# Kernel optimization log

Hardware: AMD Instinct MI355X
Metric: run time of the kernel (lower is better)

The kernel has to match this reference:

```python
import jax, jax.numpy as jnp
import numpy as np

B, T, C, H = 8, 2048, 1024, 64

def setup_inputs() -> dict:
    key = jax.random.key(0)
    k1, k2, k3, k4 = jax.random.split(key, 4)
    x = jax.random.normal(k1, (B, T, C), dtype=jnp.float32)
    s = 1.0 / np.sqrt(C)
    Wq = jax.random.normal(k2, (C, H), dtype=jnp.float32) * s
    Wk = jax.random.normal(k3, (C, H), dtype=jnp.float32) * s
    Wv = jax.random.normal(k4, (C, H), dtype=jnp.float32) * s
    return {"x": x, "Wq": Wq, "Wk": Wk, "Wv": Wv}

def reference(x, Wq, Wk, Wv):
    # single-head causal attention; note: scale uses sqrt(n_emb)=sqrt(C), as in source
    q = jnp.einsum('btc,ch->bth', x, Wq)
    k = jnp.einsum('btc,ch->bth', x, Wk)
    v = jnp.einsum('btc,ch->bth', x, Wv)
    wei = jnp.einsum('bth,bsh->bts', q, k) / jnp.sqrt(jnp.float32(C))  # [B,T,T]
    causal = jnp.tril(jnp.ones((T, T), dtype=bool))
    wei = jnp.where(causal, wei, jnp.float32(-jnp.inf))
    wei = jax.nn.softmax(wei, axis=-1)
    out = jnp.einsum('bts,bsh->bth', wei, v)  # [B,T,H]
    return out
```

## Files before the change

### kernel.cpp

```cpp
#include <hip/hip_runtime.h>

#define BT_ (8 * 2048)
#define T_  2048
#define H_  64

__global__ __launch_bounds__(256) void qkv_proj(
    const float* __restrict__ x,
    const float* __restrict__ Wq,
    const float* __restrict__ Wk,
    const float* __restrict__ Wv,
    float* __restrict__ qkv) {
  __shared__ float xT[32][68];
  __shared__ float wl[32][196];

  const int tid = threadIdx.x;
  const int tx = tid & 15;
  const int ty = tid >> 4;
  const int row0 = blockIdx.x * 64;

  float acc[4][12];
#pragma unroll
  for (int r = 0; r < 4; ++r)
#pragma unroll
    for (int c = 0; c < 12; ++c) acc[r][c] = 0.f;

  for (int kc = 0; kc < 1024; kc += 32) {
#pragma unroll
    for (int i = 0; i < 2; ++i) {
      int idx = tid + i * 256;
      int r = idx >> 3;
      int k4 = (idx & 7) * 4;
      const float4 v = *reinterpret_cast<const float4*>(
          &x[(size_t)(row0 + r) * 1024 + kc + k4]);
      xT[k4 + 0][r] = v.x;
      xT[k4 + 1][r] = v.y;
      xT[k4 + 2][r] = v.z;
      xT[k4 + 3][r] = v.w;
    }
    {
      const float* wp[3] = {Wq, Wk, Wv};
#pragma unroll
      for (int m = 0; m < 3; ++m) {
#pragma unroll
        for (int i = 0; i < 2; ++i) {
          int idx = tid + i * 256;
          int r = idx >> 4;
          int h4 = (idx & 15) * 4;
          const float4 v = *reinterpret_cast<const float4*>(
              &wp[m][(size_t)(kc + r) * 64 + h4]);
          *reinterpret_cast<float4*>(&wl[r][m * 64 + h4]) = v;
        }
      }
    }
    __syncthreads();

#pragma unroll
    for (int kk = 0; kk < 32; ++kk) {
      const float4 xv = *reinterpret_cast<const float4*>(&xT[kk][ty * 4]);
      const float4 w0 = *reinterpret_cast<const float4*>(&wl[kk][tx * 12 + 0]);
      const float4 w1 = *reinterpret_cast<const float4*>(&wl[kk][tx * 12 + 4]);
      const float4 w2 = *reinterpret_cast<const float4*>(&wl[kk][tx * 12 + 8]);
      const float xr[4] = {xv.x, xv.y, xv.z, xv.w};
      const float wr[12] = {w0.x, w0.y, w0.z, w0.w, w1.x, w1.y, w1.z, w1.w,
                            w2.x, w2.y, w2.z, w2.w};
#pragma unroll
      for (int r = 0; r < 4; ++r)
#pragma unroll
        for (int c = 0; c < 12; ++c)
          acc[r][c] = fmaf(xr[r], wr[c], acc[r][c]);
    }
    __syncthreads();
  }

#pragma unroll
  for (int r = 0; r < 4; ++r) {
#pragma unroll
    for (int g = 0; g < 3; ++g) {
      const int col = tx * 12 + g * 4;
      const int m = col >> 6;
      const int h = col & 63;
      float4 v = make_float4(acc[r][g * 4 + 0], acc[r][g * 4 + 1],
                             acc[r][g * 4 + 2], acc[r][g * 4 + 3]);
      *reinterpret_cast<float4*>(
          &qkv[(size_t)m * BT_ * H_ + (size_t)(row0 + ty * 4 + r) * H_ + h]) = v;
    }
  }
}

__global__ __launch_bounds__(256) void attn_fwd(
    const float* __restrict__ qkv, float* __restrict__ out) {
  __shared__ float qT[64][36];
  __shared__ float kT[64][68];
  __shared__ float vl[64][68];
  __shared__ float pT[64][36];

  const int tid = threadIdx.x;
  const int tx = tid & 15;
  const int ty = tid >> 4;
  const int b  = blockIdx.x & 7;
  const int qt = 63 - (blockIdx.x >> 3);
  const int r0 = qt * 32;

  const float* Q = qkv;
  const float* K = qkv + (size_t)BT_ * H_;
  const float* V = qkv + (size_t)2 * BT_ * H_;

#pragma unroll
  for (int i = 0; i < 2; ++i) {
    int idx = tid + i * 256;
    int r = idx >> 4;
    int h4 = (idx & 15) * 4;
    float4 v = *reinterpret_cast<const float4*>(
        &Q[((size_t)b * T_ + r0 + r) * H_ + h4]);
    qT[h4 + 0][r] = v.x * 0.03125f;
    qT[h4 + 1][r] = v.y * 0.03125f;
    qT[h4 + 2][r] = v.z * 0.03125f;
    qT[h4 + 3][r] = v.w * 0.03125f;
  }

  float m0 = -1e30f, m1 = -1e30f, l0 = 0.f, l1 = 0.f;
  float o0[4] = {0, 0, 0, 0}, o1[4] = {0, 0, 0, 0};

  const int nkt = qt / 2 + 1;
  for (int kt = 0; kt < nkt; ++kt) {
#pragma unroll
    for (int i = 0; i < 4; ++i) {
      int idx = tid + i * 256;
      int j = idx >> 4;
      int h4 = (idx & 15) * 4;
      size_t g = ((size_t)b * T_ + kt * 64 + j) * H_ + h4;
      float4 kv = *reinterpret_cast<const float4*>(&K[g]);
      kT[h4 + 0][j] = kv.x;
      kT[h4 + 1][j] = kv.y;
      kT[h4 + 2][j] = kv.z;
      kT[h4 + 3][j] = kv.w;
      *reinterpret_cast<float4*>(&vl[j][h4]) =
          *reinterpret_cast<const float4*>(&V[g]);
    }
    __syncthreads();

    float s0[4] = {0, 0, 0, 0}, s1[4] = {0, 0, 0, 0};
#pragma unroll
    for (int h = 0; h < 64; ++h) {
      float2 qv = *reinterpret_cast<const float2*>(&qT[h][ty * 2]);
      float4 kv = *reinterpret_cast<const float4*>(&kT[h][tx * 4]);
      const float kr[4] = {kv.x, kv.y, kv.z, kv.w};
#pragma unroll
      for (int c = 0; c < 4; ++c) {
        s0[c] = fmaf(qv.x, kr[c], s0[c]);
        s1[c] = fmaf(qv.y, kr[c], s1[c]);
      }
    }

    if (kt == nkt - 1) {
      const int rg = r0 + ty * 2;
#pragma unroll
      for (int c = 0; c < 4; ++c) {
        const int jg = kt * 64 + tx * 4 + c;
        if (jg > rg)     s0[c] = -1e30f;
        if (jg > rg + 1) s1[c] = -1e30f;
      }
    }

    float mt0 = fmaxf(fmaxf(s0[0], s0[1]), fmaxf(s0[2], s0[3]));
    float mt1 = fmaxf(fmaxf(s1[0], s1[1]), fmaxf(s1[2], s1[3]));
#pragma unroll
    for (int d = 1; d < 16; d <<= 1) {
      mt0 = fmaxf(mt0, __shfl_xor(mt0, d));
      mt1 = fmaxf(mt1, __shfl_xor(mt1, d));
    }
    const float mn0 = fmaxf(m0, mt0), mn1 = fmaxf(m1, mt1);
    const float a0 = __expf(m0 - mn0), a1 = __expf(m1 - mn1);
    float p0[4], p1[4], sum0 = 0.f, sum1 = 0.f;
#pragma unroll
    for (int c = 0; c < 4; ++c) {
      p0[c] = __expf(s0[c] - mn0);
      p1[c] = __expf(s1[c] - mn1);
      sum0 += p0[c];
      sum1 += p1[c];
    }
#pragma unroll
    for (int d = 1; d < 16; d <<= 1) {
      sum0 += __shfl_xor(sum0, d);
      sum1 += __shfl_xor(sum1, d);
    }
    l0 = l0 * a0 + sum0;
    l1 = l1 * a1 + sum1;
    m0 = mn0;
    m1 = mn1;
#pragma unroll
    for (int c = 0; c < 4; ++c) {
      o0[c] *= a0;
      o1[c] *= a1;
    }

#pragma unroll
    for (int c = 0; c < 4; ++c) {
      pT[tx * 4 + c][ty * 2 + 0] = p0[c];
      pT[tx * 4 + c][ty * 2 + 1] = p1[c];
    }
    __syncthreads();

#pragma unroll
    for (int j = 0; j < 64; ++j) {
      float2 pv = *reinterpret_cast<const float2*>(&pT[j][ty * 2]);
      float4 vv = *reinterpret_cast<const float4*>(&vl[j][tx * 4]);
      const float vr[4] = {vv.x, vv.y, vv.z, vv.w};
#pragma unroll
      for (int c = 0; c < 4; ++c) {
        o0[c] = fmaf(pv.x, vr[c], o0[c]);
        o1[c] = fmaf(pv.y, vr[c], o1[c]);
      }
    }
    __syncthreads();
  }

  const float inv0 = 1.0f / l0, inv1 = 1.0f / l1;
  const size_t orow = ((size_t)b * T_ + r0 + ty * 2) * H_ + tx * 4;
  *reinterpret_cast<float4*>(&out[orow]) =
      make_float4(o0[0] * inv0, o0[1] * inv0, o0[2] * inv0, o0[3] * inv0);
  *reinterpret_cast<float4*>(&out[orow + H_]) =
      make_float4(o1[0] * inv1, o1[1] * inv1, o1[2] * inv1, o1[3] * inv1);
}

extern "C" void kernel_launch(void* const* d_in, const int* in_sizes, int n_in,
                              void* d_out, int out_size, void* d_ws,
                              size_t ws_size, hipStream_t stream) {
  const float* x  = (const float*)d_in[0];
  const float* Wq = (const float*)d_in[1];
  const float* Wk = (const float*)d_in[2];
  const float* Wv = (const float*)d_in[3];
  float* ws  = (float*)d_ws;
  float* out = (float*)d_out;

  qkv_proj<<<256, 256, 0, stream>>>(x, Wq, Wk, Wv, ws);
  attn_fwd<<<512, 256, 0, stream>>>(ws, out);
}
```

Measured before the change: 316.3 us.

## Split long causal query tiles across KV halves and merge with combine kernel

The attention kernel now splits the 32 longest query tiles per batch into two KV-range halves. The partial outputs, max and sum are written to workspace, and a new combine kernel merges them, which balances work across 768 blocks. Each thread also computes a 4x4 register tile instead of 2x4, with 128-thread blocks and smaller shared-memory padding. The QKV projection is retiled to 32 rows per 128-thread block with partial unrolling. This adds an extra kernel launch and workspace traffic, and the changed padding may introduce LDS bank conflicts.

```diff
diff --git a/kernel.cpp b/kernel.cpp
--- a/kernel.cpp
+++ b/kernel.cpp
@@ -4,19 +4,24 @@
 #define T_  2048
 #define H_  64
 
-__global__ __launch_bounds__(256) void qkv_proj(
+#define QKV_F (3 * BT_ * H_)
+#define PO_F  QKV_F
+#define PM_F  (PO_F + 512 * 32 * 64)
+#define PL_F  (PM_F + 512 * 32)
+
+__global__ __launch_bounds__(128) void qkv_proj(
     const float* __restrict__ x,
     const float* __restrict__ Wq,
     const float* __restrict__ Wk,
     const float* __restrict__ Wv,
     float* __restrict__ qkv) {
-  __shared__ float xT[32][68];
+  __shared__ float xT[32][33];
   __shared__ float wl[32][196];
 
   const int tid = threadIdx.x;
   const int tx = tid & 15;
   const int ty = tid >> 4;
-  const int row0 = blockIdx.x * 64;
+  const int row0 = blockIdx.x * 32;
 
   float acc[4][12];
 #pragma unroll
@@ -27,7 +32,7 @@
   for (int kc = 0; kc < 1024; kc += 32) {
 #pragma unroll
     for (int i = 0; i < 2; ++i) {
-      int idx = tid + i * 256;
+      int idx = tid + i * 128;
       int r = idx >> 3;
       int k4 = (idx & 7) * 4;
       const float4 v = *reinterpret_cast<const float4*>(
@@ -42,8 +47,8 @@
 #pragma unroll
       for (int m = 0; m < 3; ++m) {
 #pragma unroll
-        for (int i = 0; i < 2; ++i) {
-          int idx = tid + i * 256;
+        for (int i = 0; i < 4; ++i) {
+          int idx = tid + i * 128;
           int r = idx >> 4;
           int h4 = (idx & 15) * 4;
           const float4 v = *reinterpret_cast<const float4*>(
@@ -54,7 +59,7 @@
     }
     __syncthreads();
 
-#pragma unroll
+#pragma unroll 8
     for (int kk = 0; kk < 32; ++kk) {
       const float4 xv = *reinterpret_cast<const float4*>(&xT[kk][ty * 4]);
       const float4 w0 = *reinterpret_cast<const float4*>(&wl[kk][tx * 12 + 0]);
@@ -87,18 +92,34 @@
   }
 }
 
-__global__ __launch_bounds__(256) void attn_fwd(
-    const float* __restrict__ qkv, float* __restrict__ out) {
-  __shared__ float qT[64][36];
-  __shared__ float kT[64][68];
-  __shared__ float vl[64][68];
-  __shared__ float pT[64][36];
+__global__ __launch_bounds__(128) void attn_fwd(
+    const float* __restrict__ qkv, float* __restrict__ out,
+    float* __restrict__ ws) {
+  __shared__ float qT[64][33];
+  __shared__ float kT[64][65];
+  __shared__ float vl[64][65];
+  __shared__ float pT[64][33];
 
   const int tid = threadIdx.x;
   const int tx = tid & 15;
   const int ty = tid >> 4;
   const int b  = blockIdx.x & 7;
-  const int qt = 63 - (blockIdx.x >> 3);
+  const int g  = blockIdx.x >> 3;
+
+  int qt, kt0, nktp, half;
+  bool masked;
+  if (g < 32) {
+    qt = 63 - g;
+    const int n = qt / 2 + 1;
+    kt0 = 0; nktp = (n + 1) / 2; masked = false; half = 0;
+  } else if (g < 64) {
+    qt = 63 - (g - 32);
+    const int n = qt / 2 + 1;
+    kt0 = (n + 1) / 2; nktp = n - kt0; masked = true; half = 1;
+  } else {
+    qt = 95 - g;
+    kt0 = 0; nktp = qt / 2 + 1; masked = true; half = -1;
+  }
   const int r0 = qt * 32;
 
   const float* Q = qkv;
@@ -106,8 +127,8 @@
   const float* V = qkv + (size_t)2 * BT_ * H_;
 
 #pragma unroll
-  for (int i = 0; i < 2; ++i) {
-    int idx = tid + i * 256;
+  for (int i = 0; i < 4; ++i) {
+    int idx = tid + i * 128;
     int r = idx >> 4;
     int h4 = (idx & 15) * 4;
     float4 v = *reinterpret_cast<const float4*>(
@@ -118,109 +139,153 @@
     qT[h4 + 3][r] = v.w * 0.03125f;
   }
 
-  float m0 = -1e30f, m1 = -1e30f, l0 = 0.f, l1 = 0.f;
-  float o0[4] = {0, 0, 0, 0}, o1[4] = {0, 0, 0, 0};
-
-  const int nkt = qt / 2 + 1;
-  for (int kt = 0; kt < nkt; ++kt) {
-#pragma unroll
-    for (int i = 0; i < 4; ++i) {
-      int idx = tid + i * 256;
+  float m[4] = {-1e30f, -1e30f, -1e30f, -1e30f};
+  float l[4] = {0, 0, 0, 0};
+  float o[4][4];
+#pragma unroll
+  for (int r = 0; r < 4; ++r)
+#pragma unroll
+    for (int c = 0; c < 4; ++c) o[r][c] = 0.f;
+
+  const int ktEnd = kt0 + nktp;
+  for (int kt = kt0; kt < ktEnd; ++kt) {
+#pragma unroll
+    for (int i = 0; i < 8; ++i) {
+      int idx = tid + i * 128;
       int j = idx >> 4;
       int h4 = (idx & 15) * 4;
-      size_t g = ((size_t)b * T_ + kt * 64 + j) * H_ + h4;
-      float4 kv = *reinterpret_cast<const float4*>(&K[g]);
+      size_t gk = ((size_t)b * T_ + kt * 64 + j) * H_ + h4;
+      float4 kv = *reinterpret_cast<const float4*>(&K[gk]);
       kT[h4 + 0][j] = kv.x;
       kT[h4 + 1][j] = kv.y;
       kT[h4 + 2][j] = kv.z;
       kT[h4 + 3][j] = kv.w;
       *reinterpret_cast<float4*>(&vl[j][h4]) =
-          *reinterpret_cast<const float4*>(&V[g]);
-    }
-    __syncthreads();
-
-    float s0[4] = {0, 0, 0, 0}, s1[4] = {0, 0, 0, 0};
-#pragma unroll
+          *reinterpret_cast<const float4*>(&V[gk]);
+    }
+    __syncthreads();
+
+    float s[4][4];
+#pragma unroll
+    for (int r = 0; r < 4; ++r)
+#pragma unroll
+      for (int c = 0; c < 4; ++c) s[r][c] = 0.f;
+#pragma unroll 8
     for (int h = 0; h < 64; ++h) {
-      float2 qv = *reinterpret_cast<const float2*>(&qT[h][ty * 2]);
-      float4 kv = *reinterpret_cast<const float4*>(&kT[h][tx * 4]);
+      const float4 qv = *reinterpret_cast<const float4*>(&qT[h][ty * 4]);
+      const float4 kv = *reinterpret_cast<const float4*>(&kT[h][tx * 4]);
+      const float qr[4] = {qv.x, qv.y, qv.z, qv.w};
       const float kr[4] = {kv.x, kv.y, kv.z, kv.w};
 #pragma unroll
+      for (int r = 0; r < 4; ++r)
+#pragma unroll
+        for (int c = 0; c < 4; ++c)
+          s[r][c] = fmaf(qr[r], kr[c], s[r][c]);
+    }
+
+    if (masked && kt == ktEnd - 1) {
+#pragma unroll
+      for (int r = 0; r < 4; ++r) {
+        const int row = r0 + ty * 4 + r;
+#pragma unroll
+        for (int c = 0; c < 4; ++c)
+          if (kt * 64 + tx * 4 + c > row) s[r][c] = -1e30f;
+      }
+    }
+
+#pragma unroll
+    for (int r = 0; r < 4; ++r) {
+      float mt = fmaxf(fmaxf(s[r][0], s[r][1]), fmaxf(s[r][2], s[r][3]));
+#pragma unroll
+      for (int d = 1; d < 16; d <<= 1) mt = fmaxf(mt, __shfl_xor(mt, d));
+      const float mn = fmaxf(m[r], mt);
+      const float a = __expf(m[r] - mn);
+      float sum = 0.f;
+#pragma unroll
       for (int c = 0; c < 4; ++c) {
-        s0[c] = fmaf(qv.x, kr[c], s0[c]);
-        s1[c] = fmaf(qv.y, kr[c], s1[c]);
+        s[r][c] = __expf(s[r][c] - mn);
+        sum += s[r][c];
       }
-    }
-
-    if (kt == nkt - 1) {
-      const int rg = r0 + ty * 2;
-#pragma unroll
-      for (int c = 0; c < 4; ++c) {
-        const int jg = kt * 64 + tx * 4 + c;
-        if (jg > rg)     s0[c] = -1e30f;
-        if (jg > rg + 1) s1[c] = -1e30f;
+#pragma unroll
+      for (int d = 1; d < 16; d <<= 1) sum += __shfl_xor(sum, d);
+      l[r] = l[r] * a + sum;
+      m[r] = mn;
+#pragma unroll
+      for (int c = 0; c < 4; ++c) o[r][c] *= a;
+    }
+
+#pragma unroll
+    for (int c = 0; c < 4; ++c) {
+      *reinterpret_cast<float4*>(&pT[tx * 4 + c][ty * 4]) =
+          make_float4(s[0][c], s[1][c], s[2][c], s[3][c]);
+    }
+    __syncthreads();
+
+#pragma unroll 8
+    for (int j = 0; j < 64; ++j) {
+      const float4 pv = *reinterpret_cast<const float4*>(&pT[j][ty * 4]);
+      const float4 vv = *reinterpret_cast<const float4*>(&vl[j][tx * 4]);
+      const float pr[4] = {pv.x, pv.y, pv.z, pv.w};
+      const float vr[4] = {vv.x, vv.y, vv.z, vv.w};
+#pragma unroll
+      for (int r = 0; r < 4; ++r)
+#pragma unroll
+        for (int c = 0; c < 4; ++c)
+          o[r][c] = fmaf(pr[r], vr[c], o[r][c]);
+    }
+    __syncthreads();
+  }
+
+  if (half < 0) {
+#pragma unroll
+    for (int r = 0; r < 4; ++r) {
+      const float inv = 1.0f / l[r];
+      *reinterpret_cast<float4*>(
+          &out[((size_t)b * T_ + r0 + ty * 4 + r) * H_ + tx * 4]) =
+          make_float4(o[r][0] * inv, o[r][1] * inv, o[r][2] * inv,
+                      o[r][3] * inv);
+    }
+  } else {
+    const int pidx = half * 256 + b * 32 + (qt - 32);
+#pragma unroll
+    for (int r = 0; r < 4; ++r) {
+      const int row = ty * 4 + r;
+      *reinterpret_cast<float4*>(
+          &ws[PO_F + ((size_t)pidx * 32 + row) * 64 + tx * 4]) =
+          make_float4(o[r][0], o[r][1], o[r][2], o[r][3]);
+      if (tx == 0) {
+        ws[PM_F + pidx * 32 + row] = m[r];
+        ws[PL_F + pidx * 32 + row] = l[r];
       }
     }
-
-    float mt0 = fmaxf(fmaxf(s0[0], s0[1]), fmaxf(s0[2], s0[3]));
-    float mt1 = fmaxf(fmaxf(s1[0], s1[1]), fmaxf(s1[2], s1[3]));
-#pragma unroll
-    for (int d = 1; d < 16; d <<= 1) {
-      mt0 = fmaxf(mt0, __shfl_xor(mt0, d));
-      mt1 = fmaxf(mt1, __shfl_xor(mt1, d));
-    }
-    const float mn0 = fmaxf(m0, mt0), mn1 = fmaxf(m1, mt1);
-    const float a0 = __expf(m0 - mn0), a1 = __expf(m1 - mn1);
-    float p0[4], p1[4], sum0 = 0.f, sum1 = 0.f;
-#pragma unroll
-    for (int c = 0; c < 4; ++c) {
-      p0[c] = __expf(s0[c] - mn0);
-      p1[c] = __expf(s1[c] - mn1);
-      sum0 += p0[c];
-      sum1 += p1[c];
-    }
-#pragma unroll
-    for (int d = 1; d < 16; d <<= 1) {
-      sum0 += __shfl_xor(sum0, d);
-      sum1 += __shfl_xor(sum1, d);
-    }
-    l0 = l0 * a0 + sum0;
-    l1 = l1 * a1 + sum1;
-    m0 = mn0;
-    m1 = mn1;
-#pragma unroll
-    for (int c = 0; c < 4; ++c) {
-      o0[c] *= a0;
-      o1[c] *= a1;
-    }
-
-#pragma unroll
-    for (int c = 0; c < 4; ++c) {
-      pT[tx * 4 + c][ty * 2 + 0] = p0[c];
-      pT[tx * 4 + c][ty * 2 + 1] = p1[c];
-    }
-    __syncthreads();
-
-#pragma unroll
-    for (int j = 0; j < 64; ++j) {
-      float2 pv = *reinterpret_cast<const float2*>(&pT[j][ty * 2]);
-      float4 vv = *reinterpret_cast<const float4*>(&vl[j][tx * 4]);
-      const float vr[4] = {vv.x, vv.y, vv.z, vv.w};
-#pragma unroll
-      for (int c = 0; c < 4; ++c) {
-        o0[c] = fmaf(pv.x, vr[c], o0[c]);
-        o1[c] = fmaf(pv.y, vr[c], o1[c]);
-      }
-    }
-    __syncthreads();
-  }
-
-  const float inv0 = 1.0f / l0, inv1 = 1.0f / l1;
-  const size_t orow = ((size_t)b * T_ + r0 + ty * 2) * H_ + tx * 4;
-  *reinterpret_cast<float4*>(&out[orow]) =
-      make_float4(o0[0] * inv0, o0[1] * inv0, o0[2] * inv0, o0[3] * inv0);
-  *reinterpret_cast<float4*>(&out[orow + H_]) =
-      make_float4(o1[0] * inv1, o1[1] * inv1, o1[2] * inv1, o1[3] * inv1);
+  }
+}
+
+__global__ __launch_bounds__(256) void attn_combine(
+    const float* __restrict__ ws, float* __restrict__ out) {
+  const int gid = blockIdx.x * 256 + threadIdx.x;
+  const int rowid = gid >> 4;
+  const int h4 = (gid & 15) * 4;
+  const int b = rowid >> 10;
+  const int rem = rowid & 1023;
+  const int qt = 32 + (rem >> 5);
+  const int r = rem & 31;
+  const int p = b * 32 + (qt - 32);
+  const int pa = p, pb = 256 + p;
+
+  const float mA = ws[PM_F + pa * 32 + r], mB = ws[PM_F + pb * 32 + r];
+  const float lA = ws[PL_F + pa * 32 + r], lB = ws[PL_F + pb * 32 + r];
+  const float mm = fmaxf(mA, mB);
+  const float sA = __expf(mA - mm), sB = __expf(mB - mm);
+  const float inv = 1.0f / (lA * sA + lB * sB);
+  const float4 oA = *reinterpret_cast<const float4*>(
+      &ws[PO_F + ((size_t)pa * 32 + r) * 64 + h4]);
+  const float4 oB = *reinterpret_cast<const float4*>(
+      &ws[PO_F + ((size_t)pb * 32 + r) * 64 + h4]);
+  *reinterpret_cast<float4*>(
+      &out[((size_t)b * T_ + qt * 32 + r) * H_ + h4]) =
+      make_float4((oA.x * sA + oB.x * sB) * inv, (oA.y * sA + oB.y * sB) * inv,
+                  (oA.z * sA + oB.z * sB) * inv, (oA.w * sA + oB.w * sB) * inv);
 }
 
 extern "C" void kernel_launch(void* const* d_in, const int* in_sizes, int n_in,
@@ -233,6 +298,7 @@
   float* ws  = (float*)d_ws;
   float* out = (float*)d_out;
 
-  qkv_proj<<<256, 256, 0, stream>>>(x, Wq, Wk, Wv, ws);
-  attn_fwd<<<512, 256, 0, stream>>>(ws, out);
+  qkv_proj<<<512, 128, 0, stream>>>(x, Wq, Wk, Wv, ws);
+  attn_fwd<<<768, 128, 0, stream>>>(ws, out, ws);
+  attn_combine<<<512, 256, 0, stream>>>(ws, out);
 }
```

New measurement: 402.8 us. 27.3% more time.
